# Optimization experiments

Hardware: AMD Instinct MI355X
Metric: run time of the kernel (lower is better)

## Reference

```python
import jax, jax.numpy as jnp
import numpy as np

N = 100000          # nodes
E = 1_600_000       # edges (before self-loops)
F_IN = 128          # input node features
H1, C1 = 8, 16      # layer-1 heads / per-head channels (concat -> 128)
NUM_CLASSES = 40
NEG_SLOPE = 0.2


def _gat_conv(x, src, dst, W, a_src, a_dst, b, concat):
    """PyG-style GATConv (eval mode, self-loops already in src/dst)."""
    n = x.shape[0]
    H, C = a_src.shape
    h = (x @ W).reshape(n, H, C)                      # [N,H,C]
    s_src = jnp.einsum('nhc,hc->nh', h, a_src)        # [N,H] per-node src logits
    s_dst = jnp.einsum('nhc,hc->nh', h, a_dst)        # [N,H] per-node dst logits
    e = jax.nn.leaky_relu(s_src[src] + s_dst[dst], NEG_SLOPE)   # [E',H]
    # segment softmax over destination node
    m = jax.ops.segment_max(e, dst, num_segments=n)   # [N,H]
    m = jnp.where(jnp.isfinite(m), m, jnp.zeros_like(m))
    p = jnp.exp(e - m[dst])                           # [E',H]
    denom = jax.ops.segment_sum(p, dst, num_segments=n)
    alpha = p / (denom[dst] + 1e-16)                  # [E',H]
    out = jax.ops.segment_sum(alpha[:, :, None] * h[src], dst, num_segments=n)  # [N,H,C]
    out = out.reshape(n, H * C) if concat else out.mean(axis=1)
    return out + b


def setup_inputs() -> dict:
    key = jax.random.key(0)
    ks = jax.random.split(key, 10)
    glorot = lambda k, shp: jax.random.normal(k, shp, jnp.float32) * np.sqrt(2.0 / (shp[0] + shp[-1] if len(shp) > 1 else shp[0]))
    return {
        'x': jax.random.normal(ks[0], (N, F_IN), jnp.float32),
        'edge_index': jax.random.randint(ks[1], (2, E), 0, N, jnp.int64),
        'W1': glorot(ks[2], (F_IN, H1 * C1)),
        'att_src1': glorot(ks[3], (H1, C1)),
        'att_dst1': glorot(ks[4], (H1, C1)),
        'b1': jnp.zeros((H1 * C1,), jnp.float32),
        'W2': glorot(ks[5], (H1 * C1, NUM_CLASSES)),
        'att_src2': glorot(ks[6], (1, NUM_CLASSES)),
        'att_dst2': glorot(ks[7], (1, NUM_CLASSES)),
        'b2': jnp.zeros((NUM_CLASSES,), jnp.float32),
    }


def reference(x, edge_index, W1, att_src1, att_dst1, b1, W2, att_src2, att_dst2, b2):
    n = x.shape[0]
    loops = jnp.arange(n, dtype=edge_index.dtype)
    src = jnp.concatenate([edge_index[0], loops])     # add self-loops (PyG default)
    dst = jnp.concatenate([edge_index[1], loops])
    h = _gat_conv(x, src, dst, W1, att_src1, att_dst1, b1, concat=True)   # [N,128]
    h = jax.nn.relu(h)
    # dropout: identity in eval mode
    out = _gat_conv(h, src, dst, W2, att_src2, att_dst2, b2, concat=True) # heads=1 -> [N,40]
    return jax.nn.log_softmax(out, axis=1)
```

## Files before the change

kernel.cpp:

```cpp
#include <hip/hip_runtime.h>
#include <math.h>

#define N_NODES 100000
#define F_IN    128
#define H1      8
#define C1      16
#define D1      128
#define NCLS    40
#define NEG     0.2f

typedef unsigned int uint32;
typedef unsigned short ushort16;

__device__ __forceinline__ ushort16 f2bf(float f) {
    unsigned int u = __float_as_uint(f);
    u += 0x7fffu + ((u >> 16) & 1u);
    return (ushort16)(u >> 16);
}
__device__ __forceinline__ float bf_lo(uint32 p) { return __uint_as_float(p << 16); }
__device__ __forceinline__ float bf_hi(uint32 p) { return __uint_as_float(p & 0xffff0000u); }

__global__ __launch_bounds__(256) void gemm1_kernel(
    const float* __restrict__ x, const float* __restrict__ W,
    uint32* __restrict__ hb,
    const float* __restrict__ a_src, const float* __restrict__ a_dst,
    float* __restrict__ ssrc, float* __restrict__ sdst)
{
    __shared__ float xs[64][132];
    const int row0 = blockIdx.x * 64;
    const int tid = threadIdx.x;
#pragma unroll
    for (int i = 0; i < 8; ++i) {
        int idx = tid + i * 256;
        int r = idx >> 5, c4 = idx & 31;
        float4 v = make_float4(0.f, 0.f, 0.f, 0.f);
        if (row0 + r < N_NODES)
            v = ((const float4*)x)[(size_t)(row0 + r) * 32 + c4];
        *(float4*)&xs[r][c4 * 4] = v;
    }
    __syncthreads();
    const int cg = tid & 15;
    const int rg = tid >> 4;
    float acc[4][8];
#pragma unroll
    for (int i = 0; i < 4; ++i)
#pragma unroll
        for (int j = 0; j < 8; ++j) acc[i][j] = 0.f;

    for (int k0 = 0; k0 < 128; k0 += 4) {
        float4 wa[4], wb[4];
#pragma unroll
        for (int kk = 0; kk < 4; ++kk) {
            wa[kk] = ((const float4*)W)[(k0 + kk) * 32 + 2 * cg];
            wb[kk] = ((const float4*)W)[(k0 + kk) * 32 + 2 * cg + 1];
        }
#pragma unroll
        for (int i = 0; i < 4; ++i) {
            float4 hx = *(const float4*)&xs[rg + 16 * i][k0];
            float hv[4] = {hx.x, hx.y, hx.z, hx.w};
#pragma unroll
            for (int kk = 0; kk < 4; ++kk) {
                acc[i][0] = fmaf(hv[kk], wa[kk].x, acc[i][0]);
                acc[i][1] = fmaf(hv[kk], wa[kk].y, acc[i][1]);
                acc[i][2] = fmaf(hv[kk], wa[kk].z, acc[i][2]);
                acc[i][3] = fmaf(hv[kk], wa[kk].w, acc[i][3]);
                acc[i][4] = fmaf(hv[kk], wb[kk].x, acc[i][4]);
                acc[i][5] = fmaf(hv[kk], wb[kk].y, acc[i][5]);
                acc[i][6] = fmaf(hv[kk], wb[kk].z, acc[i][6]);
                acc[i][7] = fmaf(hv[kk], wb[kk].w, acc[i][7]);
            }
        }
    }
    __syncthreads();
#pragma unroll
    for (int i = 0; i < 4; ++i) {
        int r = rg + 16 * i;
        uint4 pk;
        pk.x = ((uint32)f2bf(acc[i][0])) | ((uint32)f2bf(acc[i][1]) << 16);
        pk.y = ((uint32)f2bf(acc[i][2])) | ((uint32)f2bf(acc[i][3]) << 16);
        pk.z = ((uint32)f2bf(acc[i][4])) | ((uint32)f2bf(acc[i][5]) << 16);
        pk.w = ((uint32)f2bf(acc[i][6])) | ((uint32)f2bf(acc[i][7]) << 16);
        if (row0 + r < N_NODES)
            ((uint4*)hb)[(size_t)(row0 + r) * 16 + cg] = pk;
        *(float4*)&xs[r][8 * cg]     = make_float4(acc[i][0], acc[i][1], acc[i][2], acc[i][3]);
        *(float4*)&xs[r][8 * cg + 4] = make_float4(acc[i][4], acc[i][5], acc[i][6], acc[i][7]);
    }
    __syncthreads();
#pragma unroll
    for (int t = 0; t < 2; ++t) {
        int task = tid + t * 256;
        int r = task >> 3, hh = task & 7;
        if (row0 + r < N_NODES) {
            float as = 0.f, ad = 0.f;
#pragma unroll
            for (int c = 0; c < 16; ++c) {
                float v = xs[r][hh * 16 + c];
                as = fmaf(v, a_src[hh * 16 + c], as);
                ad = fmaf(v, a_dst[hh * 16 + c], ad);
            }
            ssrc[(row0 + r) * 8 + hh] = as;
            sdst[(row0 + r) * 8 + hh] = ad;
        }
    }
}

__global__ void count_kernel(const int* __restrict__ ei, int E,
                             int* __restrict__ deg,
                             int* __restrict__ rank)
{
    int e = blockIdx.x * blockDim.x + threadIdx.x;
    if (e < E) rank[e] = atomicAdd(&deg[ei[E + e]], 1);
}

__global__ void scan1_kernel(const int* __restrict__ deg,
                             int* __restrict__ incl,
                             int* __restrict__ bsum)
{
    __shared__ int tmp[256];
    int i = blockIdx.x * 256 + threadIdx.x;
    int v = (i < N_NODES) ? deg[i] : 0;
    tmp[threadIdx.x] = v;
    __syncthreads();
    for (int o = 1; o < 256; o <<= 1) {
        int t = (threadIdx.x >= (unsigned)o) ? tmp[threadIdx.x - o] : 0;
        __syncthreads();
        tmp[threadIdx.x] += t;
        __syncthreads();
    }
    if (i < N_NODES) incl[i] = tmp[threadIdx.x];
    if (threadIdx.x == 255) bsum[blockIdx.x] = tmp[255];
}

__global__ void scan2_kernel(int* __restrict__ bsum, int nb)
{
    __shared__ int tmp[512];
    int v = (threadIdx.x < (unsigned)nb) ? bsum[threadIdx.x] : 0;
    tmp[threadIdx.x] = v;
    __syncthreads();
    for (int o = 1; o < 512; o <<= 1) {
        int t = (threadIdx.x >= (unsigned)o) ? tmp[threadIdx.x - o] : 0;
        __syncthreads();
        tmp[threadIdx.x] += t;
        __syncthreads();
    }
    if (threadIdx.x < (unsigned)nb) bsum[threadIdx.x] = tmp[threadIdx.x] - v;
}

__global__ void scan3_kernel(const int* __restrict__ incl,
                             const int* __restrict__ bsum,
                             int* __restrict__ offsets)
{
    int i = blockIdx.x * 256 + threadIdx.x;
    if (i < N_NODES) offsets[i + 1] = incl[i] + bsum[blockIdx.x];
    if (i == 0) offsets[0] = 0;
}

__global__ void scatter_kernel(const int* __restrict__ ei, int E,
                               const int* __restrict__ offsets,
                               const int* __restrict__ rank,
                               int* __restrict__ srcs)
{
    int e = blockIdx.x * blockDim.x + threadIdx.x;
    if (e >= E) return;
    int s = ei[e], d = ei[E + e];
    srcs[offsets[d] + rank[e]] = s;
}

__global__ void gather1_kernel(const uint32* __restrict__ hb,
                               const float* __restrict__ ssrc,
                               const float* __restrict__ sdst,
                               const int* __restrict__ offsets,
                               const int* __restrict__ srcs,
                               const float* __restrict__ b1,
                               float* __restrict__ out)
{
    int d = (blockIdx.x * blockDim.x + threadIdx.x) >> 6;
    int lane = threadIdx.x & 63;
    if (d >= N_NODES) return;
    const int hw = lane & 7;
    const int hc = lane >> 3;
    const float sd_w = sdst[d * H1 + hw];

    float acc0 = 0.f, acc1 = 0.f;
    float wsum = 0.f;

    float ws_self;
    {
        float lg = ssrc[d * H1 + hc] + sdst[d * H1 + hc];
        lg = lg >= 0.f ? lg : NEG * lg;
        float w = __expf(lg);
        uint32 p = hb[(size_t)d * 64 + lane];
        acc0 = w * bf_lo(p); acc1 = w * bf_hi(p);
        ws_self = w;
    }

    const int beg = offsets[d], end = offsets[d + 1];
    int base = beg;
    for (; base + 8 <= end; base += 8) {
        int s_l = srcs[base + (lane >> 3)];
        float lg = ssrc[s_l * H1 + hw] + sd_w;
        lg = lg >= 0.f ? lg : NEG * lg;
        float w_l = __expf(lg);
        wsum += w_l;
#pragma unroll
        for (int j = 0; j < 8; ++j) {
            int s = __shfl(s_l, j << 3);
            float w = __shfl(w_l, (j << 3) | hc);
            uint32 p = hb[(size_t)s * 64 + lane];
            acc0 = fmaf(w, bf_lo(p), acc0);
            acc1 = fmaf(w, bf_hi(p), acc1);
        }
    }
    int cnt = end - base;
    if (cnt > 0) {
        int s_l = 0; float w_l = 0.f;
        if ((lane >> 3) < cnt) {
            s_l = srcs[base + (lane >> 3)];
            float lg = ssrc[s_l * H1 + hw] + sd_w;
            lg = lg >= 0.f ? lg : NEG * lg;
            w_l = __expf(lg);
        }
        wsum += w_l;
        for (int j = 0; j < cnt; ++j) {
            int s = __shfl(s_l, j << 3);
            float w = __shfl(w_l, (j << 3) | hc);
            uint32 p = hb[(size_t)s * 64 + lane];
            acc0 = fmaf(w, bf_lo(p), acc0);
            acc1 = fmaf(w, bf_hi(p), acc1);
        }
    }
    wsum += __shfl_xor(wsum, 8);
    wsum += __shfl_xor(wsum, 16);
    wsum += __shfl_xor(wsum, 32);
    float ws = ws_self + __shfl(wsum, hc);
    float inv = 1.f / (ws + 1e-16f);
    float2 bb = ((const float2*)b1)[lane];
    float v0 = acc0 * inv + bb.x;
    float v1 = acc1 * inv + bb.y;
    float2 r;
    r.x = v0 > 0.f ? v0 : 0.f;
    r.y = v1 > 0.f ? v1 : 0.f;
    ((float2*)(out + (size_t)d * D1))[lane] = r;
}

__global__ __launch_bounds__(256) void gemm2_kernel(
    const float* __restrict__ h, const float* __restrict__ W2,
    ushort16* __restrict__ h2b,
    const float* __restrict__ a_src, const float* __restrict__ a_dst,
    float* __restrict__ ssrc, float* __restrict__ sdst)
{
    __shared__ float w2s[40][132];
    __shared__ float hs[32][132];
    const int row0 = blockIdx.x * 32;
    const int tid = threadIdx.x;
#pragma unroll
    for (int i = 0; i < 20; ++i) {
        int idx = tid + i * 256;
        int k = idx / 40, c = idx % 40;
        w2s[c][k] = W2[idx];
    }
#pragma unroll
    for (int i = 0; i < 4; ++i) {
        int idx = tid + i * 256;
        int r = idx >> 5, c4 = idx & 31;
        *(float4*)&hs[r][c4 * 4] = ((const float4*)h)[(size_t)(row0 + r) * 32 + c4];
    }
    __syncthreads();
    const int rg = tid >> 3;
    const int g  = tid & 7;
    float acc[5] = {0.f, 0.f, 0.f, 0.f, 0.f};
    for (int k0 = 0; k0 < 128; k0 += 4) {
        float4 hv = *(const float4*)&hs[rg][k0];
#pragma unroll
        for (int j = 0; j < 5; ++j) {
            float4 wv = *(const float4*)&w2s[5 * g + j][k0];
            acc[j] = fmaf(hv.x, wv.x, acc[j]);
            acc[j] = fmaf(hv.y, wv.y, acc[j]);
            acc[j] = fmaf(hv.z, wv.z, acc[j]);
            acc[j] = fmaf(hv.w, wv.w, acc[j]);
        }
    }
#pragma unroll
    for (int j = 0; j < 5; ++j)
        h2b[(size_t)(row0 + rg) * 40 + 5 * g + j] = f2bf(acc[j]);
    __syncthreads();
#pragma unroll
    for (int j = 0; j < 5; ++j)
        hs[rg][5 * g + j] = acc[j];
    __syncthreads();
    if (tid < 32) {
        float as = 0.f, ad = 0.f;
#pragma unroll
        for (int c = 0; c < 40; ++c) {
            float v = hs[tid][c];
            as = fmaf(v, a_src[c], as);
            ad = fmaf(v, a_dst[c], ad);
        }
        ssrc[row0 + tid] = as;
        sdst[row0 + tid] = ad;
    }
}

__global__ void gather2_kernel(const uint32* __restrict__ h2b,
                               const float* __restrict__ ssrc,
                               const float* __restrict__ sdst,
                               const int* __restrict__ offsets,
                               const int* __restrict__ srcs,
                               const float* __restrict__ b2,
                               float* __restrict__ out)
{
    int d = (blockIdx.x * blockDim.x + threadIdx.x) >> 6;
    int lane = threadIdx.x & 63;
    if (d >= N_NODES) return;
    const float sd = sdst[d];
    const bool act = lane < (NCLS / 2);
    float acc0 = 0.f, acc1 = 0.f, ws = 0.f;

    {
        float lg = ssrc[d] + sd; lg = lg >= 0.f ? lg : NEG * lg;
        float w = __expf(lg);
        uint32 p = act ? h2b[(size_t)d * 20 + lane] : 0u;
        acc0 = w * bf_lo(p); acc1 = w * bf_hi(p);
        ws = w;
    }
    const int beg = offsets[d], end = offsets[d + 1];
    for (int base = beg; base < end; base += 64) {
        int cnt = end - base; if (cnt > 64) cnt = 64;
        int s_l = 0; float w_l = 0.f;
        if (lane < cnt) {
            s_l = srcs[base + lane];
            float lg = ssrc[s_l] + sd; lg = lg >= 0.f ? lg : NEG * lg;
            w_l = __expf(lg);
        }
        float t = w_l;
#pragma unroll
        for (int o = 32; o > 0; o >>= 1) t += __shfl_xor(t, o);
        ws += t;
        int j = 0;
        for (; j + 4 <= cnt; j += 4) {
            int s0 = __shfl(s_l, j),     s1 = __shfl(s_l, j + 1);
            int s2 = __shfl(s_l, j + 2), s3 = __shfl(s_l, j + 3);
            float w0 = __shfl(w_l, j),     w1 = __shfl(w_l, j + 1);
            float w2 = __shfl(w_l, j + 2), w3 = __shfl(w_l, j + 3);
            uint32 p0 = 0u, p1 = 0u, p2 = 0u, p3 = 0u;
            if (act) {
                p0 = h2b[(size_t)s0 * 20 + lane];
                p1 = h2b[(size_t)s1 * 20 + lane];
                p2 = h2b[(size_t)s2 * 20 + lane];
                p3 = h2b[(size_t)s3 * 20 + lane];
            }
            acc0 = fmaf(w0, bf_lo(p0), fmaf(w1, bf_lo(p1), fmaf(w2, bf_lo(p2), fmaf(w3, bf_lo(p3), acc0))));
            acc1 = fmaf(w0, bf_hi(p0), fmaf(w1, bf_hi(p1), fmaf(w2, bf_hi(p2), fmaf(w3, bf_hi(p3), acc1))));
        }
        for (; j < cnt; ++j) {
            int s0 = __shfl(s_l, j); float w0 = __shfl(w_l, j);
            uint32 p0 = act ? h2b[(size_t)s0 * 20 + lane] : 0u;
            acc0 = fmaf(w0, bf_lo(p0), acc0);
            acc1 = fmaf(w0, bf_hi(p0), acc1);
        }
    }
    float l0 = -INFINITY, l1 = -INFINITY;
    if (act) {
        float inv = 1.f / (ws + 1e-16f);
        l0 = acc0 * inv + b2[2 * lane];
        l1 = acc1 * inv + b2[2 * lane + 1];
    }
    float m = fmaxf(l0, l1);
#pragma unroll
    for (int o = 32; o > 0; o >>= 1) m = fmaxf(m, __shfl_xor(m, o));
    float ex = act ? (__expf(l0 - m) + __expf(l1 - m)) : 0.f;
#pragma unroll
    for (int o = 32; o > 0; o >>= 1) ex += __shfl_xor(ex, o);
    float lse = __logf(ex) + m;
    if (act) {
        float2 r; r.x = l0 - lse; r.y = l1 - lse;
        ((float2*)(out + (size_t)d * NCLS))[lane] = r;
    }
}

extern "C" void kernel_launch(void* const* d_in, const int* in_sizes, int n_in,
                              void* d_out, int out_size, void* d_ws, size_t ws_size,
                              hipStream_t stream)
{
    const float* x   = (const float*)d_in[0];
    const int*   ei  = (const int*)  d_in[1];
    const float* W1  = (const float*)d_in[2];
    const float* as1 = (const float*)d_in[3];
    const float* ad1 = (const float*)d_in[4];
    const float* b1  = (const float*)d_in[5];
    const float* W2  = (const float*)d_in[6];
    const float* as2 = (const float*)d_in[7];
    const float* ad2 = (const float*)d_in[8];
    const float* b2  = (const float*)d_in[9];
    float* out = (float*)d_out;
    const int E = in_sizes[1] / 2;

    float* ws = (float*)d_ws;
    size_t off = 0;
    uint32* h1b = (uint32*)(ws + off); off += (size_t)N_NODES * 64;
    float* h1r  = ws + off; off += (size_t)N_NODES * D1;
    float* ss1  = ws + off; off += (size_t)N_NODES * H1;
    float* sd1  = ws + off; off += (size_t)N_NODES * H1;
    uint32* h2b = (uint32*)(ws + off); off += (size_t)N_NODES * 20;
    float* ss2  = ws + off; off += N_NODES;
    float* sd2  = ws + off; off += N_NODES;
    int* ib = (int*)(ws + off);
    size_t ioff = 0;
    int* deg     = ib + ioff; ioff += N_NODES;
    int* incl    = ib + ioff; ioff += N_NODES;
    int* offsets = ib + ioff; ioff += N_NODES + 1;
    int* bsum    = ib + ioff; ioff += 512;
    int* rank    = ib + ioff; ioff += E;
    int* srcs    = ib + ioff; ioff += E;

    hipMemsetAsync(deg, 0, (size_t)N_NODES * sizeof(int), stream);

    const int nb = (N_NODES + 255) / 256;
    count_kernel<<<(E + 255) / 256, 256, 0, stream>>>(ei, E, deg, rank);
    scan1_kernel<<<nb, 256, 0, stream>>>(deg, incl, bsum);
    scan2_kernel<<<1, 512, 0, stream>>>(bsum, nb);
    scan3_kernel<<<nb, 256, 0, stream>>>(incl, bsum, offsets);
    scatter_kernel<<<(E + 255) / 256, 256, 0, stream>>>(ei, E, offsets, rank, srcs);

    gemm1_kernel<<<(N_NODES + 63) / 64, 256, 0, stream>>>(x, W1, h1b, as1, ad1, ss1, sd1);
    gather1_kernel<<<(N_NODES * 64 + 255) / 256, 256, 0, stream>>>(h1b, ss1, sd1, offsets, srcs, b1, h1r);

    gemm2_kernel<<<N_NODES / 32, 256, 0, stream>>>(h1r, W2, (ushort16*)h2b, as2, ad2, ss2, sd2);
    gather2_kernel<<<(N_NODES * 64 + 255) / 256, 256, 0, stream>>>(h2b, ss2, sd2, offsets, srcs, b2, out);
}
```

Before: 466.4 us.

## Store layer-1 features as FP8 and split gathers across half-waves

```diff
diff --git a/kernel.cpp b/kernel.cpp
--- a/kernel.cpp
+++ b/kernel.cpp
@@ -11,6 +11,7 @@
 
 typedef unsigned int uint32;
 typedef unsigned short ushort16;
+typedef float v2f __attribute__((ext_vector_type(2)));
 
 __device__ __forceinline__ ushort16 f2bf(float f) {
     unsigned int u = __float_as_uint(f);
@@ -22,7 +23,7 @@
 
 __global__ __launch_bounds__(256) void gemm1_kernel(
     const float* __restrict__ x, const float* __restrict__ W,
-    uint32* __restrict__ hb,
+    uint32* __restrict__ h8,
     const float* __restrict__ a_src, const float* __restrict__ a_dst,
     float* __restrict__ ssrc, float* __restrict__ sdst)
 {
@@ -75,13 +76,14 @@
 #pragma unroll
     for (int i = 0; i < 4; ++i) {
         int r = rg + 16 * i;
-        uint4 pk;
-        pk.x = ((uint32)f2bf(acc[i][0])) | ((uint32)f2bf(acc[i][1]) << 16);
-        pk.y = ((uint32)f2bf(acc[i][2])) | ((uint32)f2bf(acc[i][3]) << 16);
-        pk.z = ((uint32)f2bf(acc[i][4])) | ((uint32)f2bf(acc[i][5]) << 16);
-        pk.w = ((uint32)f2bf(acc[i][6])) | ((uint32)f2bf(acc[i][7]) << 16);
-        if (row0 + r < N_NODES)
-            ((uint4*)hb)[(size_t)(row0 + r) * 16 + cg] = pk;
+        int p0 = __builtin_amdgcn_cvt_pk_fp8_f32(acc[i][0], acc[i][1], 0, false);
+        p0     = __builtin_amdgcn_cvt_pk_fp8_f32(acc[i][2], acc[i][3], p0, true);
+        int p1 = __builtin_amdgcn_cvt_pk_fp8_f32(acc[i][4], acc[i][5], 0, false);
+        p1     = __builtin_amdgcn_cvt_pk_fp8_f32(acc[i][6], acc[i][7], p1, true);
+        if (row0 + r < N_NODES) {
+            uint2 pk; pk.x = (uint32)p0; pk.y = (uint32)p1;
+            ((uint2*)h8)[(size_t)(row0 + r) * 16 + cg] = pk;
+        }
         *(float4*)&xs[r][8 * cg]     = make_float4(acc[i][0], acc[i][1], acc[i][2], acc[i][3]);
         *(float4*)&xs[r][8 * cg + 4] = make_float4(acc[i][4], acc[i][5], acc[i][6], acc[i][7]);
     }
@@ -166,7 +168,7 @@
     srcs[offsets[d] + rank[e]] = s;
 }
 
-__global__ void gather1_kernel(const uint32* __restrict__ hb,
+__global__ void gather1_kernel(const uint32* __restrict__ h8,
                                const float* __restrict__ ssrc,
                                const float* __restrict__ sdst,
                                const int* __restrict__ offsets,
@@ -178,20 +180,24 @@
     int lane = threadIdx.x & 63;
     if (d >= N_NODES) return;
     const int hw = lane & 7;
-    const int hc = lane >> 3;
+    const int half = lane >> 5;
+    const int u = lane & 31;
+    const int hc = u >> 2;
     const float sd_w = sdst[d * H1 + hw];
 
-    float acc0 = 0.f, acc1 = 0.f;
+    float acc0 = 0.f, acc1 = 0.f, acc2 = 0.f, acc3 = 0.f;
     float wsum = 0.f;
 
-    float ws_self;
+    float lgs = ssrc[d * H1 + hc] + sdst[d * H1 + hc];
+    lgs = lgs >= 0.f ? lgs : NEG * lgs;
+    const float ws_self = __expf(lgs);
     {
-        float lg = ssrc[d * H1 + hc] + sdst[d * H1 + hc];
-        lg = lg >= 0.f ? lg : NEG * lg;
-        float w = __expf(lg);
-        uint32 p = hb[(size_t)d * 64 + lane];
-        acc0 = w * bf_lo(p); acc1 = w * bf_hi(p);
-        ws_self = w;
+        float m = (half == 0) ? ws_self : 0.f;
+        uint32 p = h8[(size_t)d * 32 + u];
+        v2f lo = __builtin_amdgcn_cvt_pk_f32_fp8((int)p, false);
+        v2f hi = __builtin_amdgcn_cvt_pk_f32_fp8((int)p, true);
+        acc0 = m * lo[0]; acc1 = m * lo[1];
+        acc2 = m * hi[0]; acc3 = m * hi[1];
     }
 
     const int beg = offsets[d], end = offsets[d + 1];
@@ -203,12 +209,17 @@
         float w_l = __expf(lg);
         wsum += w_l;
 #pragma unroll
-        for (int j = 0; j < 8; ++j) {
+        for (int t = 0; t < 4; ++t) {
+            int j = 2 * t + half;
             int s = __shfl(s_l, j << 3);
             float w = __shfl(w_l, (j << 3) | hc);
-            uint32 p = hb[(size_t)s * 64 + lane];
-            acc0 = fmaf(w, bf_lo(p), acc0);
-            acc1 = fmaf(w, bf_hi(p), acc1);
+            uint32 p = h8[(size_t)s * 32 + u];
+            v2f lo = __builtin_amdgcn_cvt_pk_f32_fp8((int)p, false);
+            v2f hi = __builtin_amdgcn_cvt_pk_f32_fp8((int)p, true);
+            acc0 = fmaf(w, lo[0], acc0);
+            acc1 = fmaf(w, lo[1], acc1);
+            acc2 = fmaf(w, hi[0], acc2);
+            acc3 = fmaf(w, hi[1], acc3);
         }
     }
     int cnt = end - base;
@@ -221,26 +232,38 @@
             w_l = __expf(lg);
         }
         wsum += w_l;
-        for (int j = 0; j < cnt; ++j) {
+        int steps = (cnt + 1) >> 1;
+        for (int t = 0; t < steps; ++t) {
+            int j = 2 * t + half;
             int s = __shfl(s_l, j << 3);
             float w = __shfl(w_l, (j << 3) | hc);
-            uint32 p = hb[(size_t)s * 64 + lane];
-            acc0 = fmaf(w, bf_lo(p), acc0);
-            acc1 = fmaf(w, bf_hi(p), acc1);
+            uint32 p = h8[(size_t)s * 32 + u];
+            v2f lo = __builtin_amdgcn_cvt_pk_f32_fp8((int)p, false);
+            v2f hi = __builtin_amdgcn_cvt_pk_f32_fp8((int)p, true);
+            acc0 = fmaf(w, lo[0], acc0);
+            acc1 = fmaf(w, lo[1], acc1);
+            acc2 = fmaf(w, hi[0], acc2);
+            acc3 = fmaf(w, hi[1], acc3);
         }
     }
     wsum += __shfl_xor(wsum, 8);
     wsum += __shfl_xor(wsum, 16);
     wsum += __shfl_xor(wsum, 32);
     float ws = ws_self + __shfl(wsum, hc);
-    float inv = 1.f / (ws + 1e-16f);
-    float2 bb = ((const float2*)b1)[lane];
-    float v0 = acc0 * inv + bb.x;
-    float v1 = acc1 * inv + bb.y;
-    float2 r;
-    r.x = v0 > 0.f ? v0 : 0.f;
-    r.y = v1 > 0.f ? v1 : 0.f;
-    ((float2*)(out + (size_t)d * D1))[lane] = r;
+    acc0 += __shfl_xor(acc0, 32);
+    acc1 += __shfl_xor(acc1, 32);
+    acc2 += __shfl_xor(acc2, 32);
+    acc3 += __shfl_xor(acc3, 32);
+    if (half == 0) {
+        float inv = 1.f / (ws + 1e-16f);
+        float4 bb = ((const float4*)b1)[u];
+        float4 r;
+        r.x = fmaf(acc0, inv, bb.x); r.x = r.x > 0.f ? r.x : 0.f;
+        r.y = fmaf(acc1, inv, bb.y); r.y = r.y > 0.f ? r.y : 0.f;
+        r.z = fmaf(acc2, inv, bb.z); r.z = r.z > 0.f ? r.z : 0.f;
+        r.w = fmaf(acc3, inv, bb.w); r.w = r.w > 0.f ? r.w : 0.f;
+        ((float4*)(out + (size_t)d * D1))[u] = r;
+    }
 }
 
 __global__ __launch_bounds__(256) void gemm2_kernel(
@@ -313,6 +336,8 @@
     int lane = threadIdx.x & 63;
     if (d >= N_NODES) return;
     const float sd = sdst[d];
+    const int g = lane / 20;
+    const int c = lane - 20 * g;
     const bool act = lane < (NCLS / 2);
     float acc0 = 0.f, acc1 = 0.f, ws = 0.f;
 
@@ -320,7 +345,8 @@
         float lg = ssrc[d] + sd; lg = lg >= 0.f ? lg : NEG * lg;
         float w = __expf(lg);
         uint32 p = act ? h2b[(size_t)d * 20 + lane] : 0u;
-        acc0 = w * bf_lo(p); acc1 = w * bf_hi(p);
+        float m = act ? w : 0.f;
+        acc0 = m * bf_lo(p); acc1 = m * bf_hi(p);
         ws = w;
     }
     const int beg = offsets[d], end = offsets[d + 1];
@@ -336,34 +362,25 @@
 #pragma unroll
         for (int o = 32; o > 0; o >>= 1) t += __shfl_xor(t, o);
         ws += t;
-        int j = 0;
-        for (; j + 4 <= cnt; j += 4) {
-            int s0 = __shfl(s_l, j),     s1 = __shfl(s_l, j + 1);
-            int s2 = __shfl(s_l, j + 2), s3 = __shfl(s_l, j + 3);
-            float w0 = __shfl(w_l, j),     w1 = __shfl(w_l, j + 1);
-            float w2 = __shfl(w_l, j + 2), w3 = __shfl(w_l, j + 3);
-            uint32 p0 = 0u, p1 = 0u, p2 = 0u, p3 = 0u;
-            if (act) {
-                p0 = h2b[(size_t)s0 * 20 + lane];
-                p1 = h2b[(size_t)s1 * 20 + lane];
-                p2 = h2b[(size_t)s2 * 20 + lane];
-                p3 = h2b[(size_t)s3 * 20 + lane];
-            }
-            acc0 = fmaf(w0, bf_lo(p0), fmaf(w1, bf_lo(p1), fmaf(w2, bf_lo(p2), fmaf(w3, bf_lo(p3), acc0))));
-            acc1 = fmaf(w0, bf_hi(p0), fmaf(w1, bf_hi(p1), fmaf(w2, bf_hi(p2), fmaf(w3, bf_hi(p3), acc1))));
-        }
-        for (; j < cnt; ++j) {
-            int s0 = __shfl(s_l, j); float w0 = __shfl(w_l, j);
-            uint32 p0 = act ? h2b[(size_t)s0 * 20 + lane] : 0u;
-            acc0 = fmaf(w0, bf_lo(p0), acc0);
-            acc1 = fmaf(w0, bf_hi(p0), acc1);
-        }
-    }
+        for (int j = 0; j < cnt; j += 3) {
+            int jj = j + g;
+            int s = __shfl(s_l, jj & 63);
+            float w = __shfl(w_l, jj & 63);
+            if (g >= 3 || jj >= cnt) w = 0.f;
+            uint32 p = h2b[(size_t)s * 20 + c];
+            acc0 = fmaf(w, bf_lo(p), acc0);
+            acc1 = fmaf(w, bf_hi(p), acc1);
+        }
+    }
+    float r00 = __shfl(acc0, lane + 20), r01 = __shfl(acc0, lane + 40);
+    float r10 = __shfl(acc1, lane + 20), r11 = __shfl(acc1, lane + 40);
     float l0 = -INFINITY, l1 = -INFINITY;
     if (act) {
+        acc0 += r00 + r01;
+        acc1 += r10 + r11;
         float inv = 1.f / (ws + 1e-16f);
-        l0 = acc0 * inv + b2[2 * lane];
-        l1 = acc1 * inv + b2[2 * lane + 1];
+        l0 = fmaf(acc0, inv, b2[2 * lane]);
+        l1 = fmaf(acc1, inv, b2[2 * lane + 1]);
     }
     float m = fmaxf(l0, l1);
 #pragma unroll
@@ -397,7 +414,7 @@
 
     float* ws = (float*)d_ws;
     size_t off = 0;
-    uint32* h1b = (uint32*)(ws + off); off += (size_t)N_NODES * 64;
+    uint32* h1f8 = (uint32*)(ws + off); off += (size_t)N_NODES * 32;
     float* h1r  = ws + off; off += (size_t)N_NODES * D1;
     float* ss1  = ws + off; off += (size_t)N_NODES * H1;
     float* sd1  = ws + off; off += (size_t)N_NODES * H1;
@@ -422,8 +439,8 @@
     scan3_kernel<<<nb, 256, 0, stream>>>(incl, bsum, offsets);
     scatter_kernel<<<(E + 255) / 256, 256, 0, stream>>>(ei, E, offsets, rank, srcs);
 
-    gemm1_kernel<<<(N_NODES + 63) / 64, 256, 0, stream>>>(x, W1, h1b, as1, ad1, ss1, sd1);
-    gather1_kernel<<<(N_NODES * 64 + 255) / 256, 256, 0, stream>>>(h1b, ss1, sd1, offsets, srcs, b1, h1r);
+    gemm1_kernel<<<(N_NODES + 63) / 64, 256, 0, stream>>>(x, W1, h1f8, as1, ad1, ss1, sd1);
+    gather1_kernel<<<(N_NODES * 64 + 255) / 256, 256, 0, stream>>>(h1f8, ss1, sd1, offsets, srcs, b1, h1r);
 
     gemm2_kernel<<<N_NODES / 32, 256, 0, stream>>>(h1r, W2, (ushort16*)h2b, as2, ad2, ss2, sd2);
     gather2_kernel<<<(N_NODES * 64 + 255) / 256, 256, 0, stream>>>(h2b, ss2, sd2, offsets, srcs, b2, out);
```

New measurement: 424.2 us. 9.0% less time.
